# Kernel optimization log

Measured on AMD Instinct MI355X. Metric: run time of the kernel, lower is better.

## Reference

```python
import jax, jax.numpy as jnp
import numpy as np

N = 8192
IN_F = 512
OUT_F = 512
ALPHA = 0.2  # leaky relu slope


def setup_inputs() -> dict:
    key = jax.random.key(0)
    k1, k2, k3, k4, k5 = jax.random.split(key, 5)
    inp = jax.random.normal(k1, (N, IN_F), dtype=jnp.float32)
    adj = jax.random.randint(k2, (N, N), 0, 2, dtype=jnp.int32)
    # linear1: [in, out] + bias
    W1 = jax.random.normal(k3, (IN_F, OUT_F), dtype=jnp.float32) * (1.0 / np.sqrt(IN_F))
    b1 = jnp.zeros((OUT_F,), dtype=jnp.float32)
    # linear2: maps 2*out -> 1; split into the two halves acting on h_i and h_j
    a = jax.random.normal(k4, (2 * OUT_F,), dtype=jnp.float32) * (1.0 / np.sqrt(2 * OUT_F))
    a1 = a[:OUT_F]
    a2 = a[OUT_F:]
    b2 = jnp.zeros((), dtype=jnp.float32)
    return {"inp": inp, "adj": adj, "W1": W1, "b1": b1, "a1": a1, "a2": a2, "b2": b2}


def reference(inp, adj, W1, b1, a1, a2, b2):
    h = inp @ W1 + b1  # [N, out]
    # linear2(cat(h_i, h_j)) == h_i@a1 + h_j@a2 + b2 -> avoids the N*N*2F tensor
    e = jax.nn.leaky_relu((h @ a1)[:, None] + (h @ a2)[None, :] + b2, ALPHA)  # [N, N]
    attention = jnp.where(adj > 0, e, jnp.float32(-1e12))
    attention = jax.nn.softmax(attention, axis=1)
    h_prime = attention @ h  # [N, out]
    return jax.nn.elu(h_prime)  # concat=True
```

## Files before the change

### kernel.cpp

```cpp
#include <hip/hip_runtime.h>
#include <hip/hip_bf16.h>
#include <stdint.h>

#define NR 8192
#define FD 512
#define BM 64

typedef __attribute__((ext_vector_type(8))) short s8v;
typedef __attribute__((ext_vector_type(4))) float f32x4;

static __device__ __forceinline__ short bf16_rtne(float x) {
    union { float f; uint32_t u; } v; v.f = x;
    uint32_t r = (v.u + 0x7FFFu + ((v.u >> 16) & 1u)) >> 16;
    return (short)r;
}
static __device__ __forceinline__ float bf16_to_f32(short s) {
    union { uint32_t u; float f; } v; v.u = ((uint32_t)(uint16_t)s) << 16;
    return v.f;
}

__global__ void k_prepack(const int* __restrict__ adj,
                          unsigned long long* __restrict__ bm) {
    const int lane = threadIdx.x & 63;
    const int wv   = threadIdx.x >> 6;
    const int gid  = blockIdx.x * 4 + wv;
    const int row  = gid >> 2;
    const int seg  = (gid & 3) * 2048;
    const int* p   = adj + (size_t)row * NR + seg + lane;
    unsigned long long* o = bm + (((size_t)row * NR + seg) >> 6);
#pragma unroll
    for (int g = 0; g < 8; ++g) {
        unsigned long long b0 = __ballot(p[g * 256]       != 0);
        unsigned long long b1 = __ballot(p[g * 256 + 64]  != 0);
        unsigned long long b2 = __ballot(p[g * 256 + 128] != 0);
        unsigned long long b3 = __ballot(p[g * 256 + 192] != 0);
        unsigned long long vs = (lane == 0) ? b0 : (lane == 1) ? b1
                              : (lane == 2) ? b2 : b3;
        if (lane < 4) o[g * 4 + lane] = vs;
    }
}

__global__ void k_convert(const float* __restrict__ in, short* __restrict__ out) {
    int i = blockIdx.x * blockDim.x + threadIdx.x;
    float4 v = ((const float4*)in)[i];
    short4 s;
    s.x = bf16_rtne(v.x); s.y = bf16_rtne(v.y);
    s.z = bf16_rtne(v.z); s.w = bf16_rtne(v.w);
    ((short4*)out)[i] = s;
}

__global__ void k_w1t(const float* __restrict__ W1, short* __restrict__ W1T) {
    int i = blockIdx.x * 256 + threadIdx.x;
    int k = i & 511, n = i >> 9;
    W1T[(size_t)n * 512 + k] = bf16_rtne(W1[(size_t)k * 512 + n]);
}

__launch_bounds__(256)
__global__ void k_gemm_h(const short* __restrict__ A,
                         const short* __restrict__ BT,
                         const float* __restrict__ b1,
                         short* __restrict__ H,
                         short* __restrict__ HT3)
{
    const int lane = threadIdx.x & 63;
    const int wn   = threadIdx.x >> 6;
    const int m    = lane & 15;
    const int q    = lane >> 4;
    const int r0   = blockIdx.x * 32;
    const int c0   = blockIdx.y * 128 + wn * 32;

    f32x4 acc[2][2] = {};
#pragma unroll 1
    for (int k0 = 0; k0 < 512; k0 += 32) {
        s8v a[2], b[2];
#pragma unroll
        for (int rt = 0; rt < 2; ++rt)
            a[rt] = *(const s8v*)(A + (size_t)(r0 + rt * 16 + m) * 512 + k0 + q * 8);
#pragma unroll
        for (int nt = 0; nt < 2; ++nt)
            b[nt] = *(const s8v*)(BT + (size_t)(c0 + nt * 16 + m) * 512 + k0 + q * 8);
#pragma unroll
        for (int rt = 0; rt < 2; ++rt)
#pragma unroll
            for (int nt = 0; nt < 2; ++nt)
                acc[rt][nt] = __builtin_amdgcn_mfma_f32_16x16x32_bf16(a[rt], b[nt], acc[rt][nt], 0, 0, 0);
    }
    float b1v[2];
#pragma unroll
    for (int nt = 0; nt < 2; ++nt) b1v[nt] = b1[c0 + nt * 16 + m];

#pragma unroll
    for (int rt = 0; rt < 2; ++rt)
#pragma unroll
        for (int nt = 0; nt < 2; ++nt) {
            int col = c0 + nt * 16 + m;
            short4 hp;
#pragma unroll
            for (int r = 0; r < 4; ++r) {
                int row = r0 + rt * 16 + q * 4 + r;
                short hv = bf16_rtne(acc[rt][nt][r] + b1v[nt]);
                H[(size_t)row * 512 + col] = hv;
                ((short*)&hp)[r] = hv;
            }
            size_t off = (size_t)blockIdx.x * 16384
                       + (size_t)(blockIdx.y * 2 + (wn >> 1)) * 2048
                       + (size_t)((wn * 2 + nt) & 3) * 512
                       + (rt * 2 + (q >> 1)) * 128
                       + m * 8 + (q & 1) * 4;
            *(short4*)(HT3 + off) = hp;
        }
}

__global__ void k_f1f2(const short* __restrict__ H, const float* __restrict__ a1,
                       const float* __restrict__ a2, const float* __restrict__ b2,
                       float* __restrict__ f1, float* __restrict__ f2s)
{
    const int lane = threadIdx.x & 63;
    const int row  = blockIdx.x * 4 + (threadIdx.x >> 6);
    s8v hv = *(const s8v*)(H + (size_t)row * 512 + lane * 8);
    float4 a1l = ((const float4*)(a1 + lane * 8))[0];
    float4 a1h = ((const float4*)(a1 + lane * 8))[1];
    float4 a2l = ((const float4*)(a2 + lane * 8))[0];
    float4 a2h = ((const float4*)(a2 + lane * 8))[1];
    float hf[8];
#pragma unroll
    for (int i = 0; i < 8; ++i) hf[i] = bf16_to_f32(hv[i]);
    float s1 = hf[0] * a1l.x + hf[1] * a1l.y + hf[2] * a1l.z + hf[3] * a1l.w
             + hf[4] * a1h.x + hf[5] * a1h.y + hf[6] * a1h.z + hf[7] * a1h.w;
    float s2 = hf[0] * a2l.x + hf[1] * a2l.y + hf[2] * a2l.z + hf[3] * a2l.w
             + hf[4] * a2h.x + hf[5] * a2h.y + hf[6] * a2h.z + hf[7] * a2h.w;
#pragma unroll
    for (int o = 32; o > 0; o >>= 1) {
        s1 += __shfl_xor(s1, o);
        s2 += __shfl_xor(s2, o);
    }
    if (lane == 0) {
        f1[row]  = s1;
        f2s[row] = s2 + b2[0];
    }
}

__launch_bounds__(512, 2)
__global__ void k_attn(const uint32_t* __restrict__ bm,
                       const short* __restrict__ HT3,
                       const float* __restrict__ f1,
                       const float* __restrict__ f2s,
                       float* __restrict__ nump,
                       float* __restrict__ denomp)
{
    __shared__ __align__(16) short wt[2][BM * 256];

    const int t    = threadIdx.x;
    const int lane = t & 63;
    const int w    = t >> 6;
    const int m    = lane & 15;
    const int q    = lane >> 4;

    const int js   = blockIdx.x & 1;
    const int band = blockIdx.x >> 1;
    const int r0   = band * BM;
    const int jb0  = js * 4096;
    const int jt0  = js * 128;

    const int prow = t >> 3;
    const int jg   = t & 7;

    const float f1v = f1[r0 + prow];
    const uint32_t* bmrow = bm + (size_t)(r0 + prow) * 256 + js * 128;
    const float* f2base = f2s + jb0;

    f32x4 acc[4][4] = {};
    float dsum = 0.f;

#define GAT_BLOAD(DST, KT)                                                     \
    {                                                                          \
        const short* s_ = HT3 + (size_t)(jt0 + (KT)) * 16384 + w * 2048        \
                        + q * 128 + m * 8;                                     \
        DST[0] = *(const s8v*)(s_);                                            \
        DST[1] = *(const s8v*)(s_ + 512);                                      \
        DST[2] = *(const s8v*)(s_ + 1024);                                     \
        DST[3] = *(const s8v*)(s_ + 1536);                                     \
    }

#define GAT_WUNIT(U, BYTE, FA, FB, P)                                          \
    {                                                                          \
        s8v wv_;                                                               \
        const float* ff_ = (const float*)&(FA);                                \
        _Pragma("unroll")                                                      \
        for (int jj = 0; jj < 4; ++jj) {                                       \
            float s_ = f1v + ff_[jj];                                          \
            float e_ = __expf(fmaxf(s_, 0.2f * s_));                           \
            float x_ = (((BYTE) >> jj) & 1u) ? e_ : 0.f;                       \
            dsum += x_; wv_[jj] = bf16_rtne(x_);                               \
        }                                                                      \
        const float* fg_ = (const float*)&(FB);                               \
        _Pragma("unroll")                                                      \
        for (int jj = 0; jj < 4; ++jj) {                                       \
            float s_ = f1v + fg_[jj];                                          \
            float e_ = __expf(fmaxf(s_, 0.2f * s_));                           \
            float x_ = (((BYTE) >> (4 + jj)) & 1u) ? e_ : 0.f;                 \
            dsum += x_; wv_[4 + jj] = bf16_rtne(x_);                           \
        }                                                                      \
        *(s8v*)&wt[P][prow * 256 + (((U) ^ (prow & 7)) << 3)] = wv_;           \
    }

    {
        uint4 mwa_ = *(const uint4*)(bmrow);
        uint4 mwb_ = *(const uint4*)(bmrow + 4);
        uint32_t m8_[8] = {mwa_.x, mwa_.y, mwa_.z, mwa_.w,
                           mwb_.x, mwb_.y, mwb_.z, mwb_.w};
#pragma unroll
        for (int k_ = 0; k_ < 4; ++k_) {
            const int u_ = jg + 8 * k_;
            uint32_t byte_ = (m8_[(jg >> 2) + 2 * k_] >> ((jg & 3) * 8)) & 0xFFu;
            float4 fa_ = *(const float4*)(f2base + u_ * 8);
            float4 fb_ = *(const float4*)(f2base + u_ * 8 + 4);
            GAT_WUNIT(u_, byte_, fa_, fb_, 0)
        }
    }
    s8v breg[2][4];
    GAT_BLOAD(breg[0], 0)
    GAT_BLOAD(breg[1], 1)
    __syncthreads();

    int kt = 0;
#pragma unroll 1
    for (int ch = 0; ch < 16; ++ch) {
        const int p = ch & 1;
        const int chn = (ch + 1) & 15;
        uint4 mwa_ = *(const uint4*)(bmrow + chn * 8);
        uint4 mwb_ = *(const uint4*)(bmrow + chn * 8 + 4);
        float4 fa_[4], fb_[4];
#pragma unroll
        for (int k_ = 0; k_ < 4; ++k_) {
            const int u_ = jg + 8 * k_;
            fa_[k_] = *(const float4*)(f2base + chn * 256 + u_ * 8);
            fb_[k_] = *(const float4*)(f2base + chn * 256 + u_ * 8 + 4);
        }
        uint32_t m8_[8] = {mwa_.x, mwa_.y, mwa_.z, mwa_.w,
                           mwb_.x, mwb_.y, mwb_.z, mwb_.w};

#pragma unroll
        for (int kk = 0; kk < 8; ++kk, ++kt) {
            const int e = kk & 1;
            s8v bn[4];
            GAT_BLOAD(bn, (kt + 2) & 127)
            s8v af[4];
#pragma unroll
            for (int i = 0; i < 4; ++i)
                af[i] = *(const s8v*)&wt[p][(i * 16 + m) * 256
                                            + (((kk * 4 + q) ^ (m & 7)) << 3)];
#pragma unroll
            for (int nt = 0; nt < 4; ++nt)
#pragma unroll
                for (int i = 0; i < 4; ++i)
                    acc[i][nt] = __builtin_amdgcn_mfma_f32_16x16x32_bf16(af[i], breg[e][nt], acc[i][nt], 0, 0, 0);
            if (kk >= 2 && kk <= 5 && ch < 15) {
                const int k_ = kk - 2;
                const int u_ = jg + 8 * k_;
                uint32_t byte_ = (m8_[(jg >> 2) + 2 * k_] >> ((jg & 3) * 8)) & 0xFFu;
                GAT_WUNIT(u_, byte_, fa_[k_], fb_[k_], p ^ 1)
            }
#pragma unroll
            for (int nt = 0; nt < 4; ++nt) breg[e][nt] = bn[nt];
        }
        __syncthreads();
    }
#undef GAT_BLOAD
#undef GAT_WUNIT

    dsum += __shfl_xor(dsum, 1);
    dsum += __shfl_xor(dsum, 2);
    dsum += __shfl_xor(dsum, 4);
    if (jg == 0) denomp[(size_t)js * NR + r0 + prow] = dsum;

    float* np = nump + (size_t)js * NR * FD;
#pragma unroll
    for (int i = 0; i < 4; ++i)
#pragma unroll
        for (int nt = 0; nt < 4; ++nt)
#pragma unroll
            for (int r = 0; r < 4; ++r) {
                int row = r0 + i * 16 + q * 4 + r;
                int col = w * 64 + nt * 16 + m;
                np[(size_t)row * FD + col] = acc[i][nt][r];
            }
}

__global__ void k_combine(const float* __restrict__ nump,
                          const float* __restrict__ denomp,
                          float* __restrict__ out)
{
    size_t e = ((size_t)blockIdx.x * 256 + threadIdx.x) * 4;
    int row = (int)(e >> 9);
    float4 n0 = *(const float4*)(nump + e);
    float4 n1 = *(const float4*)(nump + (size_t)NR * FD + e);
    float d = denomp[row] + denomp[NR + row];
    float inv = 1.0f / d;
    float4 o;
    o.x = (n0.x + n1.x) * inv;
    o.y = (n0.y + n1.y) * inv;
    o.z = (n0.z + n1.z) * inv;
    o.w = (n0.w + n1.w) * inv;
    o.x = (o.x > 0.f) ? o.x : (__expf(o.x) - 1.f);
    o.y = (o.y > 0.f) ? o.y : (__expf(o.y) - 1.f);
    o.z = (o.z > 0.f) ? o.z : (__expf(o.z) - 1.f);
    o.w = (o.w > 0.f) ? o.w : (__expf(o.w) - 1.f);
    *(float4*)(out + e) = o;
}

extern "C" void kernel_launch(void* const* d_in, const int* in_sizes, int n_in,
                              void* d_out, int out_size, void* d_ws, size_t ws_size,
                              hipStream_t stream) {
    const float* inp = (const float*)d_in[0];
    const int*   adj = (const int*)d_in[1];
    const float* W1  = (const float*)d_in[2];
    const float* b1  = (const float*)d_in[3];
    const float* a1  = (const float*)d_in[4];
    const float* a2  = (const float*)d_in[5];
    const float* b2  = (const float*)d_in[6];
    float* out = (float*)d_out;

    short*    inp_bf = (short*)d_ws;
    short*    w1t    = inp_bf + (size_t)NR * FD;
    short*    h      = w1t + (size_t)FD * FD;
    short*    ht3    = h + (size_t)NR * FD;
    uint32_t* bmw    = (uint32_t*)(ht3 + (size_t)FD * NR);
    float*    f1     = (float*)(bmw + (size_t)NR * 256);
    float*    f2s    = f1 + NR;
    float*    nump   = f2s + NR;
    float*    denomp = nump + (size_t)2 * NR * FD;

    k_prepack<<<NR, 256, 0, stream>>>(adj, (unsigned long long*)bmw);
    k_convert<<<(NR * FD / 4) / 256, 256, 0, stream>>>(inp, inp_bf);
    k_w1t<<<(FD * FD) / 256, 256, 0, stream>>>(W1, w1t);
    dim3 g1(NR / 32, FD / 128);
    k_gemm_h<<<g1, 256, 0, stream>>>(inp_bf, w1t, b1, h, ht3);
    k_f1f2<<<NR / 4, 256, 0, stream>>>(h, a1, a2, b2, f1, f2s);
    k_attn<<<128 * 2, 512, 0, stream>>>(bmw, ht3, f1, f2s, nump, denomp);
    k_combine<<<(NR * FD / 4) / 256, 256, 0, stream>>>(nump, denomp, out);
}
```

Before: 505.0 us.

## Split attention key range four ways and stream mask/f2 loads per step

The attention kernel now splits the key dimension into four slices instead of two, launching 512 blocks, and requests 4 blocks per CU via launch bounds. This is meant to fill more CUs and raise occupancy. The bulk preload of mask words and f2 values for the next chunk is replaced by per-step loads into small register buffers, which lowers register pressure so the higher occupancy target can fit. The cost is doubled partial numerator traffic: four 8192x512 fp32 partials are written and then summed in the combine kernel, and the workspace grows to match.

```diff
diff --git a/kernel.cpp b/kernel.cpp
--- a/kernel.cpp
+++ b/kernel.cpp
@@ -140,7 +140,7 @@
     }
 }
 
-__launch_bounds__(512, 2)
+__launch_bounds__(512, 4)
 __global__ void k_attn(const uint32_t* __restrict__ bm,
                        const short* __restrict__ HT3,
                        const float* __restrict__ f1,
@@ -156,17 +156,17 @@
     const int m    = lane & 15;
     const int q    = lane >> 4;
 
-    const int js   = blockIdx.x & 1;
-    const int band = blockIdx.x >> 1;
+    const int js   = blockIdx.x & 3;
+    const int band = blockIdx.x >> 2;
     const int r0   = band * BM;
-    const int jb0  = js * 4096;
-    const int jt0  = js * 128;
+    const int jb0  = js * 2048;
+    const int jt0  = js * 64;
 
     const int prow = t >> 3;
     const int jg   = t & 7;
 
     const float f1v = f1[r0 + prow];
-    const uint32_t* bmrow = bm + (size_t)(r0 + prow) * 256 + js * 128;
+    const uint32_t* bmrow = bm + (size_t)(r0 + prow) * 256 + js * 64;
     const float* f2base = f2s + jb0;
 
     f32x4 acc[4][4] = {};
@@ -205,14 +205,11 @@
     }
 
     {
-        uint4 mwa_ = *(const uint4*)(bmrow);
-        uint4 mwb_ = *(const uint4*)(bmrow + 4);
-        uint32_t m8_[8] = {mwa_.x, mwa_.y, mwa_.z, mwa_.w,
-                           mwb_.x, mwb_.y, mwb_.z, mwb_.w};
 #pragma unroll
         for (int k_ = 0; k_ < 4; ++k_) {
             const int u_ = jg + 8 * k_;
-            uint32_t byte_ = (m8_[(jg >> 2) + 2 * k_] >> ((jg & 3) * 8)) & 0xFFu;
+            uint32_t wd_ = bmrow[(jg >> 2) + 2 * k_];
+            uint32_t byte_ = (wd_ >> ((jg & 3) * 8)) & 0xFFu;
             float4 fa_ = *(const float4*)(f2base + u_ * 8);
             float4 fb_ = *(const float4*)(f2base + u_ * 8 + 4);
             GAT_WUNIT(u_, byte_, fa_, fb_, 0)
@@ -223,28 +220,18 @@
     GAT_BLOAD(breg[1], 1)
     __syncthreads();
 
+    uint32_t wu_mask[2];
+    float4   wu_fa[2], wu_fb[2];
+
     int kt = 0;
 #pragma unroll 1
-    for (int ch = 0; ch < 16; ++ch) {
+    for (int ch = 0; ch < 8; ++ch) {
         const int p = ch & 1;
-        const int chn = (ch + 1) & 15;
-        uint4 mwa_ = *(const uint4*)(bmrow + chn * 8);
-        uint4 mwb_ = *(const uint4*)(bmrow + chn * 8 + 4);
-        float4 fa_[4], fb_[4];
-#pragma unroll
-        for (int k_ = 0; k_ < 4; ++k_) {
-            const int u_ = jg + 8 * k_;
-            fa_[k_] = *(const float4*)(f2base + chn * 256 + u_ * 8);
-            fb_[k_] = *(const float4*)(f2base + chn * 256 + u_ * 8 + 4);
-        }
-        uint32_t m8_[8] = {mwa_.x, mwa_.y, mwa_.z, mwa_.w,
-                           mwb_.x, mwb_.y, mwb_.z, mwb_.w};
-
 #pragma unroll
         for (int kk = 0; kk < 8; ++kk, ++kt) {
             const int e = kk & 1;
             s8v bn[4];
-            GAT_BLOAD(bn, (kt + 2) & 127)
+            GAT_BLOAD(bn, (kt + 2) & 63)
             s8v af[4];
 #pragma unroll
             for (int i = 0; i < 4; ++i)
@@ -255,11 +242,17 @@
 #pragma unroll
                 for (int i = 0; i < 4; ++i)
                     acc[i][nt] = __builtin_amdgcn_mfma_f32_16x16x32_bf16(af[i], breg[e][nt], acc[i][nt], 0, 0, 0);
-            if (kk >= 2 && kk <= 5 && ch < 15) {
-                const int k_ = kk - 2;
+            if (kk >= 2 && kk <= 5 && ch < 7) {
+                const int u_ = jg + 8 * (kk - 2);
+                uint32_t byte_ = (wu_mask[e] >> ((jg & 3) * 8)) & 0xFFu;
+                GAT_WUNIT(u_, byte_, wu_fa[e], wu_fb[e], p ^ 1)
+            }
+            if (kk < 4 && ch < 7) {
+                const int k_ = kk;
                 const int u_ = jg + 8 * k_;
-                uint32_t byte_ = (m8_[(jg >> 2) + 2 * k_] >> ((jg & 3) * 8)) & 0xFFu;
-                GAT_WUNIT(u_, byte_, fa_[k_], fb_[k_], p ^ 1)
+                wu_mask[e] = bmrow[(ch + 1) * 8 + (jg >> 2) + 2 * k_];
+                wu_fa[e] = *(const float4*)(f2base + (ch + 1) * 256 + u_ * 8);
+                wu_fb[e] = *(const float4*)(f2base + (ch + 1) * 256 + u_ * 8 + 4);
             }
 #pragma unroll
             for (int nt = 0; nt < 4; ++nt) breg[e][nt] = bn[nt];
@@ -295,13 +288,15 @@
     int row = (int)(e >> 9);
     float4 n0 = *(const float4*)(nump + e);
     float4 n1 = *(const float4*)(nump + (size_t)NR * FD + e);
-    float d = denomp[row] + denomp[NR + row];
+    float4 n2 = *(const float4*)(nump + (size_t)2 * NR * FD + e);
+    float4 n3 = *(const float4*)(nump + (size_t)3 * NR * FD + e);
+    float d = denomp[row] + denomp[NR + row] + denomp[2 * NR + row] + denomp[3 * NR + row];
     float inv = 1.0f / d;
     float4 o;
-    o.x = (n0.x + n1.x) * inv;
-    o.y = (n0.y + n1.y) * inv;
-    o.z = (n0.z + n1.z) * inv;
-    o.w = (n0.w + n1.w) * inv;
+    o.x = (n0.x + n1.x + n2.x + n3.x) * inv;
+    o.y = (n0.y + n1.y + n2.y + n3.y) * inv;
+    o.z = (n0.z + n1.z + n2.z + n3.z) * inv;
+    o.w = (n0.w + n1.w + n2.w + n3.w) * inv;
     o.x = (o.x > 0.f) ? o.x : (__expf(o.x) - 1.f);
     o.y = (o.y > 0.f) ? o.y : (__expf(o.y) - 1.f);
     o.z = (o.z > 0.f) ? o.z : (__expf(o.z) - 1.f);
@@ -329,7 +324,7 @@
     float*    f1     = (float*)(bmw + (size_t)NR * 256);
     float*    f2s    = f1 + NR;
     float*    nump   = f2s + NR;
-    float*    denomp = nump + (size_t)2 * NR * FD;
+    float*    denomp = nump + (size_t)4 * NR * FD;
 
     k_prepack<<<NR, 256, 0, stream>>>(adj, (unsigned long long*)bmw);
     k_convert<<<(NR * FD / 4) / 256, 256, 0, stream>>>(inp, inp_bf);
@@ -337,6 +332,6 @@
     dim3 g1(NR / 32, FD / 128);
     k_gemm_h<<<g1, 256, 0, stream>>>(inp_bf, w1t, b1, h, ht3);
     k_f1f2<<<NR / 4, 256, 0, stream>>>(h, a1, a2, b2, f1, f2s);
-    k_attn<<<128 * 2, 512, 0, stream>>>(bmw, ht3, f1, f2s, nump, denomp);
+    k_attn<<<128 * 4, 512, 0, stream>>>(bmw, ht3, f1, f2s, nump, denomp);
     k_combine<<<(NR * FD / 4) / 256, 256, 0, stream>>>(nump, denomp, out);
 }
```

New measurement: 633.9 us. +25.5%, slower.
